# Performance work log

Hardware: AMD Instinct MI355X
Metric: run time of the kernel (lower is better)

## Reference

```python
import jax, jax.numpy as jnp
import numpy as np

EPSILON = 1e-8

def setup_inputs() -> dict:
    key = jax.random.key(0)
    k1, k2, k3, k4 = jax.random.split(key, 4)
    B, C_in, C_out, H, W, S, K = 16, 512, 512, 32, 32, 512, 3
    x = jax.random.normal(k1, (B, C_in, H, W), dtype=jnp.float32)
    w = jax.random.normal(k2, (B, S), dtype=jnp.float32)
    # Linear(style_dim -> in_chan), bias initialized to ones per module code
    style_w = jax.random.normal(k3, (C_in, S), dtype=jnp.float32) * (1.0 / np.sqrt(S))
    style_b = jnp.ones((C_in,), dtype=jnp.float32)
    # kaiming_normal_(fan_in, leaky_relu): std = sqrt(2/(1+0.01^2)) / sqrt(fan_in)
    fan_in = C_in * K * K
    gain = np.sqrt(2.0 / (1.0 + 0.01 ** 2))
    weight = jax.random.normal(k4, (C_out, C_in, K, K), dtype=jnp.float32) * (gain / np.sqrt(fan_in))
    return {"x": x, "w": w, "style_w": style_w, "style_b": style_b, "weight": weight}

def reference(x, w, style_w, style_b, weight):
    B, C, H, W_ = x.shape
    C_out, _, K, _ = weight.shape
    # style modulation: Linear(style_dim -> in_chan)
    style = w @ style_w.T + style_b                       # (B, C_in)
    weights = style[:, None, :, None, None] * weight[None]  # (B, C_out, C_in, K, K)
    # demodulation
    d = jax.lax.rsqrt(jnp.sum(weights * weights, axis=(2, 3, 4), keepdims=True) + EPSILON)
    weights = weights * d
    # grouped conv with groups = batch
    pad = 1 if K > 1 else 0
    xg = x.reshape(1, B * C, H, W_)
    wg = weights.reshape(B * C_out, C, K, K)
    y = jax.lax.conv_general_dilated(
        xg, wg, window_strides=(1, 1), padding=((pad, pad), (pad, pad)),
        dimension_numbers=("NCHW", "OIHW", "NCHW"), feature_group_count=B)
    return y.reshape(B, C_out, H, W_)
```

## Files before the change

kernel.cpp:

```cpp
#include <hip/hip_runtime.h>
#include <hip/hip_bf16.h>

#define NB 16
#define CI 512
#define CO 512
#define HW 1024
#define SD 512
#define EPSI 1e-8f

typedef __attribute__((ext_vector_type(8))) short bf16x8;
typedef __attribute__((ext_vector_type(16))) float f32x16;
typedef __attribute__((ext_vector_type(4))) unsigned int u32x4;

#define GLOAD_LDS16(g, l) __builtin_amdgcn_global_load_lds( \
    (const __attribute__((address_space(1))) unsigned int*)(const void*)(g), \
    (__attribute__((address_space(3))) unsigned int*)(void*)(l), 16, 0, 0)
#define SCHED0() __builtin_amdgcn_sched_barrier(0)
#define SBAR()   __builtin_amdgcn_s_barrier()

__global__ void k_style2(const float* __restrict__ w, const float* __restrict__ sw,
                         const float* __restrict__ sb, float* __restrict__ style) {
    int gw = (blockIdx.x * 256 + threadIdx.x) >> 6;
    int l = threadIdx.x & 63;
    int b = gw >> 9, c = gw & 511;
    const float4* wr = (const float4*)(w + b * SD) + (l << 1);
    const float4* sr = (const float4*)(sw + c * SD) + (l << 1);
    float4 a0 = wr[0], a1 = wr[1], q0 = sr[0], q1 = sr[1];
    float acc = a0.x * q0.x + a0.y * q0.y + a0.z * q0.z + a0.w * q0.w
              + a1.x * q1.x + a1.y * q1.y + a1.z * q1.z + a1.w * q1.w;
#pragma unroll
    for (int off = 32; off > 0; off >>= 1) acc += __shfl_down(acc, off);
    if (l == 0) style[gw] = acc + sb[c];
}

__global__ void k_wprep(const float* __restrict__ wt, float* __restrict__ wsq,
                        __hip_bfloat16* __restrict__ wtb, u32x4* __restrict__ zpage) {
    if (blockIdx.x == 0 && threadIdx.x < 64)
        zpage[threadIdx.x] = (u32x4){0, 0, 0, 0};
    int idx = blockIdx.x * 256 + threadIdx.x;
    const float* p = wt + idx * 9;
    float a = 0.f;
#pragma unroll
    for (int t = 0; t < 9; ++t) {
        float v = p[t];
        a += v * v;
        wtb[t * (CO * CI) + idx] = __float2bfloat16(v);
    }
    wsq[idx] = a;
}

__global__ void k_demod2(const float* __restrict__ style, const float* __restrict__ wsq,
                         float* __restrict__ dv) {
    int gw = (blockIdx.x * 256 + threadIdx.x) >> 6;
    int l = threadIdx.x & 63;
    int b = gw >> 9, co = gw & 511;
    const float4* st = (const float4*)(style + b * CI) + (l << 1);
    const float4* wq = (const float4*)(wsq + co * CI) + (l << 1);
    float4 s0 = st[0], s1 = st[1], q0 = wq[0], q1 = wq[1];
    float acc = s0.x * s0.x * q0.x + s0.y * s0.y * q0.y + s0.z * s0.z * q0.z + s0.w * s0.w * q0.w
              + s1.x * s1.x * q1.x + s1.y * s1.y * q1.y + s1.z * s1.z * q1.z + s1.w * s1.w * q1.w;
#pragma unroll
    for (int off = 32; off > 0; off >>= 1) acc += __shfl_down(acc, off);
    if (l == 0) dv[gw] = rsqrtf(acc + EPSI);
}

__global__ void k_xs(const float* __restrict__ x, const float* __restrict__ style,
                     __hip_bfloat16* __restrict__ xs) {
    __shared__ float tile[32][33];
    int b = blockIdx.z, c0 = blockIdx.y * 32, p0 = blockIdx.x * 32;
    int tx = threadIdx.x & 31, ty = threadIdx.x >> 5;
#pragma unroll
    for (int i = 0; i < 4; ++i) {
        int ci = c0 + ty + i * 8;
        tile[ty + i * 8][tx] = x[(b * CI + ci) * HW + p0 + tx] * style[b * CI + ci];
    }
    __syncthreads();
#pragma unroll
    for (int i = 0; i < 4; ++i) {
        int p = p0 + ty + i * 8;
        xs[(b * HW + p) * CI + c0 + tx] = __float2bfloat16(tile[tx][ty + i * 8]);
    }
}

#define XS_BYTES 26112
#define WBUF_BYTES 16384
#define SMEM_TOTAL (XS_BYTES + 3 * WBUF_BYTES)

extern "C" __global__ __launch_bounds__(256, 2) void k_conv(
        const __hip_bfloat16* __restrict__ wtb,
        const __hip_bfloat16* __restrict__ xs,
        const float* __restrict__ dvec,
        const char* __restrict__ zpage,
        float* __restrict__ out) {
    extern __shared__ char smem[];
    char* Xs  = smem;
    char* Wsb = smem + XS_BYTES;

    const int tid  = threadIdx.x;
    const int lane = tid & 63;
    const int wv   = tid >> 6;
    const int wr   = wv >> 1;
    const int wn   = wv & 1;

    int bid = blockIdx.x;
    int xcd = bid & 7, idx = bid >> 3;
    const int cot = xcd >> 1;
    const int px8 = idx & 7;
    const int b   = (idx >> 3) | ((xcd & 1) << 3);
    const int co0 = cot * 128;
    const int p0  = px8 * 128;
    const int y0  = px8 * 4;

    if (tid < 96) {
        int g = tid & 7;
        int rx = (tid & 8) ? 33 : 0;
        int row = tid >> 4;
        *(u32x4*)(Xs + (row * 34 + rx) * 128 + g * 16) = (u32x4){0, 0, 0, 0};
    }

    const int srcgW = (lane & 7) ^ (lane >> 3);

    auto issueW = [&](int tap, int cin, int bufi) {
        const __hip_bfloat16* wsrc = wtb + ((size_t)tap * CO + co0) * CI + cin;
        char* wdst = Wsb + bufi * WBUF_BYTES;
#pragma unroll
        for (int k = 0; k < 4; ++k) {
            int seg = k * 4 + wv;
            int co_l = seg * 8 + (lane >> 3);
            GLOAD_LDS16(wsrc + co_l * CI + srcgW * 8, wdst + seg * 1024);
        }
    };
    auto issueX = [&](int cin) {
#pragma unroll
        for (int k = 0; k < 6; ++k) {
            int sid = k * 4 + wv;
            int ry = sid >> 2, seg = sid & 3;
            int rx0 = 1 + seg * 8;
            char* ldst = Xs + (ry * 34 + rx0) * 128;
            int y = y0 - 1 + ry;
            int rx = rx0 + (lane >> 3);
            int srcg = (lane & 7) ^ (rx & 7);
            if ((unsigned)y < 32u)
                GLOAD_LDS16(xs + ((size_t)b * HW + (y << 5) + (rx - 1)) * CI + cin + srcg * 8, ldst);
            else
                GLOAD_LDS16(zpage, ldst);
        }
    };

    f32x16 acc[2][2];
#pragma unroll
    for (int m = 0; m < 2; ++m)
#pragma unroll
        for (int n = 0; n < 2; ++n)
            acc[m][n] = (f32x16)(0.f);

    issueW(0, 0, 0);
    issueW(1, 0, 1);
    issueX(0);
    SCHED0();
    asm volatile("s_waitcnt lgkmcnt(0) vmcnt(0)" ::: "memory");
    SCHED0();
    SBAR();
    SCHED0();

    for (int cc = 0; cc < 8; ++cc) {
#pragma unroll
        for (int t = 0; t < 9; ++t) {
            if (!(cc == 7 && t >= 7)) {
                const int tn  = (t <= 6) ? (t + 2) : (t - 7);
                const int cin = ((t <= 6) ? cc : (cc + 1)) * 64;
                issueW(tn, cin, (t + 2) % 3);
            }
            SCHED0();

            const char* Wb = Wsb + (t % 3) * WBUF_BYTES;
            const int ky = t / 3, kx = t - (t / 3) * 3;
            __builtin_amdgcn_s_setprio(1);
#pragma unroll
            for (int q = 0; q < 4; ++q) {
                bf16x8 afr[2], bfr[2];
                int g = (q << 1) + (lane >> 5);
#pragma unroll
                for (int m = 0; m < 2; ++m) {
                    int cr = wr * 64 + m * 32 + (lane & 31);
                    afr[m] = *(const bf16x8*)(Wb + cr * 128 + ((g ^ (cr & 7)) << 4));
                }
#pragma unroll
                for (int n = 0; n < 2; ++n) {
                    int ry = wn * 2 + n + ky;
                    int rx = (lane & 31) + kx;
                    bfr[n] = *(const bf16x8*)(Xs + ((ry * 34 + rx) * 128) +
                                              ((g ^ (rx & 7)) << 4));
                }
#pragma unroll
                for (int m = 0; m < 2; ++m)
#pragma unroll
                    for (int n = 0; n < 2; ++n)
                        acc[m][n] = __builtin_amdgcn_mfma_f32_32x32x16_bf16(afr[m], bfr[n], acc[m][n], 0, 0, 0);
            }
            __builtin_amdgcn_s_setprio(0);

            if (cc == 7 && t == 8) {
            } else if (t == 8) {
                SCHED0();
                asm volatile("s_waitcnt lgkmcnt(0)" ::: "memory");
                SCHED0();
                SBAR();
                SCHED0();
                issueX((cc + 1) * 64);
                SCHED0();
                asm volatile("s_waitcnt lgkmcnt(0) vmcnt(0)" ::: "memory");
                SCHED0();
                SBAR();
                SCHED0();
            } else if (cc == 7 && t == 7) {
                SCHED0();
                asm volatile("s_waitcnt lgkmcnt(0) vmcnt(0)" ::: "memory");
                SCHED0();
                SBAR();
                SCHED0();
            } else {
                SCHED0();
                asm volatile("s_waitcnt lgkmcnt(0) vmcnt(4)" ::: "memory");
                SCHED0();
                SBAR();
                SCHED0();
            }
        }
    }

#pragma unroll
    for (int m = 0; m < 2; ++m) {
#pragma unroll
        for (int r = 0; r < 16; ++r) {
            int co = co0 + wr * 64 + m * 32 + (r & 3) + ((r >> 2) << 3) + ((lane >> 5) << 2);
            float dvv = dvec[b * CO + co];
            float* orow = out + ((size_t)b * CO + co) * HW + p0 + wn * 64;
            orow[lane & 31]        = acc[m][0][r] * dvv;
            orow[32 + (lane & 31)] = acc[m][1][r] * dvv;
        }
    }
}

extern "C" void kernel_launch(void* const* d_in, const int* in_sizes, int n_in,
                              void* d_out, int out_size, void* d_ws, size_t ws_size,
                              hipStream_t stream) {
    const float* x  = (const float*)d_in[0];
    const float* w  = (const float*)d_in[1];
    const float* sw = (const float*)d_in[2];
    const float* sb = (const float*)d_in[3];
    const float* wt = (const float*)d_in[4];
    float* out = (float*)d_out;

    char* ws = (char*)d_ws;
    float* style = (float*)(ws);
    float* dvec  = (float*)(ws + 32768);
    float* wsq   = (float*)(ws + 65536);
    __hip_bfloat16* wtb = (__hip_bfloat16*)(ws + 1114112);
    __hip_bfloat16* xsb = (__hip_bfloat16*)(ws + 5832704);
    char* zpage = ws + 22609920;

    hipFuncSetAttribute((const void*)k_conv,
                        hipFuncAttributeMaxDynamicSharedMemorySize, SMEM_TOTAL);

    k_style2<<<2048, 256, 0, stream>>>(w, sw, sb, style);
    k_wprep<<<1024, 256, 0, stream>>>(wt, wsq, (__hip_bfloat16*)wtb, (u32x4*)zpage);
    k_xs<<<dim3(32, 16, 16), 256, 0, stream>>>(x, style, xsb);
    k_demod2<<<2048, 256, 0, stream>>>(style, wsq, dvec);
    k_conv<<<512, 256, SMEM_TOTAL, stream>>>(wtb, xsb, dvec, zpage, out);
}
```

Baseline: 99.90 us.

## Fuse demodulation into conv, split K across waves, widen xs transpose

Drops the separate demod kernel and computes the per-output-channel demod factors inside the conv prologue into LDS. The conv's wave decomposition changes from a 2x2 M/N split to a split of the K dimension across wave pairs, with a final LDS reduction before the store. The pipeline schedule is restructured so the X tile load is issued at the start of each channel chunk. The xs transpose kernel now handles 64 channels per block and writes 16-byte vectors. These changes aim to cut a kernel launch and increase A-fragment reuse per wave, at the cost of more accumulator registers and an extra reduction pass.

```diff
diff --git a/kernel.cpp b/kernel.cpp
--- a/kernel.cpp
+++ b/kernel.cpp
@@ -49,58 +49,48 @@
     wsq[idx] = a;
 }
 
-__global__ void k_demod2(const float* __restrict__ style, const float* __restrict__ wsq,
-                         float* __restrict__ dv) {
-    int gw = (blockIdx.x * 256 + threadIdx.x) >> 6;
-    int l = threadIdx.x & 63;
-    int b = gw >> 9, co = gw & 511;
-    const float4* st = (const float4*)(style + b * CI) + (l << 1);
-    const float4* wq = (const float4*)(wsq + co * CI) + (l << 1);
-    float4 s0 = st[0], s1 = st[1], q0 = wq[0], q1 = wq[1];
-    float acc = s0.x * s0.x * q0.x + s0.y * s0.y * q0.y + s0.z * s0.z * q0.z + s0.w * s0.w * q0.w
-              + s1.x * s1.x * q1.x + s1.y * s1.y * q1.y + s1.z * s1.z * q1.z + s1.w * s1.w * q1.w;
-#pragma unroll
-    for (int off = 32; off > 0; off >>= 1) acc += __shfl_down(acc, off);
-    if (l == 0) dv[gw] = rsqrtf(acc + EPSI);
-}
-
 __global__ void k_xs(const float* __restrict__ x, const float* __restrict__ style,
                      __hip_bfloat16* __restrict__ xs) {
-    __shared__ float tile[32][33];
-    int b = blockIdx.z, c0 = blockIdx.y * 32, p0 = blockIdx.x * 32;
+    __shared__ float tile[32][66];
+    int b = blockIdx.z, c0 = blockIdx.y * 64, p0 = blockIdx.x * 32;
     int tx = threadIdx.x & 31, ty = threadIdx.x >> 5;
 #pragma unroll
-    for (int i = 0; i < 4; ++i) {
-        int ci = c0 + ty + i * 8;
-        tile[ty + i * 8][tx] = x[(b * CI + ci) * HW + p0 + tx] * style[b * CI + ci];
+    for (int i = 0; i < 8; ++i) {
+        int ci = i * 8 + ty;
+        tile[tx][ci] = x[((size_t)b * CI + c0 + ci) * HW + p0 + tx] * style[b * CI + c0 + ci];
     }
     __syncthreads();
-#pragma unroll
-    for (int i = 0; i < 4; ++i) {
-        int p = p0 + ty + i * 8;
-        xs[(b * HW + p) * CI + c0 + tx] = __float2bfloat16(tile[tx][ty + i * 8]);
-    }
+    int r = threadIdx.x >> 3, kc = threadIdx.x & 7;
+    union { bf16x8 v; __hip_bfloat16 h[8]; } U;
+#pragma unroll
+    for (int i = 0; i < 8; ++i)
+        U.h[i] = __float2bfloat16(tile[r][kc * 8 + i]);
+    *(bf16x8*)(xs + ((size_t)b * HW + p0 + r) * CI + c0 + kc * 8) = U.v;
 }
 
 #define XS_BYTES 26112
-#define WBUF_BYTES 16384
-#define SMEM_TOTAL (XS_BYTES + 3 * WBUF_BYTES)
+#define WBUF 16384
+#define DV_OFF (XS_BYTES + 3 * WBUF)
+#define SMEM_TOTAL (DV_OFF + 512)
 
 extern "C" __global__ __launch_bounds__(256, 2) void k_conv(
         const __hip_bfloat16* __restrict__ wtb,
         const __hip_bfloat16* __restrict__ xs,
-        const float* __restrict__ dvec,
+        const float* __restrict__ style,
+        const float* __restrict__ wsq,
         const char* __restrict__ zpage,
         float* __restrict__ out) {
     extern __shared__ char smem[];
     char* Xs  = smem;
     char* Wsb = smem + XS_BYTES;
+    float* dvLDS = (float*)(smem + DV_OFF);
 
     const int tid  = threadIdx.x;
     const int lane = tid & 63;
+    const int l31  = lane & 31;
     const int wv   = tid >> 6;
-    const int wr   = wv >> 1;
-    const int wn   = wv & 1;
+    const int kh   = wv & 1;
+    const int wpx  = wv >> 1;
 
     int bid = blockIdx.x;
     int xcd = bid & 7, idx = bid >> 3;
@@ -122,20 +112,20 @@
 
     auto issueW = [&](int tap, int cin, int bufi) {
         const __hip_bfloat16* wsrc = wtb + ((size_t)tap * CO + co0) * CI + cin;
-        char* wdst = Wsb + bufi * WBUF_BYTES;
+        char* wdst = Wsb + bufi * WBUF;
 #pragma unroll
         for (int k = 0; k < 4; ++k) {
-            int seg = k * 4 + wv;
-            int co_l = seg * 8 + (lane >> 3);
-            GLOAD_LDS16(wsrc + co_l * CI + srcgW * 8, wdst + seg * 1024);
+            int u = k * 4 + wv;
+            int co_l = u * 8 + (lane >> 3);
+            GLOAD_LDS16(wsrc + co_l * CI + srcgW * 8, wdst + u * 1024);
         }
     };
     auto issueX = [&](int cin) {
 #pragma unroll
         for (int k = 0; k < 6; ++k) {
-            int sid = k * 4 + wv;
-            int ry = sid >> 2, seg = sid & 3;
-            int rx0 = 1 + seg * 8;
+            int u = k * 4 + wv;
+            int ry = u >> 2, q4 = u & 3;
+            int rx0 = 1 + q4 * 8;
             char* ldst = Xs + (ry * 34 + rx0) * 128;
             int y = y0 - 1 + ry;
             int rx = rx0 + (lane >> 3);
@@ -147,9 +137,9 @@
         }
     };
 
-    f32x16 acc[2][2];
-#pragma unroll
-    for (int m = 0; m < 2; ++m)
+    f32x16 acc[4][2];
+#pragma unroll
+    for (int m = 0; m < 4; ++m)
 #pragma unroll
         for (int n = 0; n < 2; ++n)
             acc[m][n] = (f32x16)(0.f);
@@ -157,6 +147,19 @@
     issueW(0, 0, 0);
     issueW(1, 0, 1);
     issueX(0);
+    {
+        int j = tid >> 1, h = tid & 1;
+        const float4* wq = (const float4*)(wsq + (size_t)(co0 + j) * CI + h * 256);
+        const float4* st = (const float4*)(style + b * CI + h * 256);
+        float a = 0.f;
+#pragma unroll 4
+        for (int i = 0; i < 64; ++i) {
+            float4 q = wq[i], s = st[i];
+            a += s.x * s.x * q.x + s.y * s.y * q.y + s.z * s.z * q.z + s.w * s.w * q.w;
+        }
+        a += __shfl_down(a, 1);
+        if (!h) dvLDS[j] = rsqrtf(a + EPSI);
+    }
     SCHED0();
     asm volatile("s_waitcnt lgkmcnt(0) vmcnt(0)" ::: "memory");
     SCHED0();
@@ -166,78 +169,101 @@
     for (int cc = 0; cc < 8; ++cc) {
 #pragma unroll
         for (int t = 0; t < 9; ++t) {
-            if (!(cc == 7 && t >= 7)) {
-                const int tn  = (t <= 6) ? (t + 2) : (t - 7);
-                const int cin = ((t <= 6) ? cc : (cc + 1)) * 64;
-                issueW(tn, cin, (t + 2) % 3);
-            }
-            SCHED0();
-
-            const char* Wb = Wsb + (t % 3) * WBUF_BYTES;
-            const int ky = t / 3, kx = t - (t / 3) * 3;
-            __builtin_amdgcn_s_setprio(1);
-#pragma unroll
-            for (int q = 0; q < 4; ++q) {
-                bf16x8 afr[2], bfr[2];
-                int g = (q << 1) + (lane >> 5);
-#pragma unroll
-                for (int m = 0; m < 2; ++m) {
-                    int cr = wr * 64 + m * 32 + (lane & 31);
-                    afr[m] = *(const bf16x8*)(Wb + cr * 128 + ((g ^ (cr & 7)) << 4));
-                }
-#pragma unroll
-                for (int n = 0; n < 2; ++n) {
-                    int ry = wn * 2 + n + ky;
-                    int rx = (lane & 31) + kx;
-                    bfr[n] = *(const bf16x8*)(Xs + ((ry * 34 + rx) * 128) +
-                                              ((g ^ (rx & 7)) << 4));
-                }
-#pragma unroll
-                for (int m = 0; m < 2; ++m)
-#pragma unroll
-                    for (int n = 0; n < 2; ++n)
-                        acc[m][n] = __builtin_amdgcn_mfma_f32_32x32x16_bf16(afr[m], bfr[n], acc[m][n], 0, 0, 0);
-            }
-            __builtin_amdgcn_s_setprio(0);
-
-            if (cc == 7 && t == 8) {
-            } else if (t == 8) {
-                SCHED0();
-                asm volatile("s_waitcnt lgkmcnt(0)" ::: "memory");
-                SCHED0();
-                SBAR();
-                SCHED0();
-                issueX((cc + 1) * 64);
-                SCHED0();
-                asm volatile("s_waitcnt lgkmcnt(0) vmcnt(0)" ::: "memory");
-                SCHED0();
-                SBAR();
-                SCHED0();
-            } else if (cc == 7 && t == 7) {
-                SCHED0();
-                asm volatile("s_waitcnt lgkmcnt(0) vmcnt(0)" ::: "memory");
-                SCHED0();
-                SBAR();
-                SCHED0();
-            } else {
+            const int s = cc * 9 + t;
+            if (t == 0 && cc > 0)
+                issueX(cc * 64);
+            if (s <= 69) {
+                const int s2 = s + 2;
+                issueW(s2 % 9, (s2 / 9) * 64, s2 % 3);
+            }
+            if (t == 0 && cc > 0) {
                 SCHED0();
                 asm volatile("s_waitcnt lgkmcnt(0) vmcnt(4)" ::: "memory");
                 SCHED0();
                 SBAR();
                 SCHED0();
             }
-        }
-    }
-
-#pragma unroll
-    for (int m = 0; m < 2; ++m) {
-#pragma unroll
-        for (int r = 0; r < 16; ++r) {
-            int co = co0 + wr * 64 + m * 32 + (r & 3) + ((r >> 2) << 3) + ((lane >> 5) << 2);
-            float dvv = dvec[b * CO + co];
-            float* orow = out + ((size_t)b * CO + co) * HW + p0 + wn * 64;
-            orow[lane & 31]        = acc[m][0][r] * dvv;
-            orow[32 + (lane & 31)] = acc[m][1][r] * dvv;
+
+            const char* Wb = Wsb + (t % 3) * WBUF;
+            const int ky = t / 3, kx = t - (t / 3) * 3;
+            __builtin_amdgcn_s_setprio(1);
+#pragma unroll
+            for (int ql = 0; ql < 2; ++ql) {
+                int g = kh * 4 + ql * 2 + (lane >> 5);
+                bf16x8 afr[4], bfr[2];
+#pragma unroll
+                for (int m = 0; m < 4; ++m) {
+                    int cr = m * 32 + l31;
+                    afr[m] = *(const bf16x8*)(Wb + cr * 128 + ((g ^ (cr & 7)) << 4));
+                }
+#pragma unroll
+                for (int n = 0; n < 2; ++n) {
+                    int row = wpx * 2 + n + ky;
+                    int rx = l31 + kx;
+                    bfr[n] = *(const bf16x8*)(Xs + (row * 34 + rx) * 128 + ((g ^ (rx & 7)) << 4));
+                }
+#pragma unroll
+                for (int m = 0; m < 4; ++m)
+#pragma unroll
+                    for (int n = 0; n < 2; ++n)
+                        acc[m][n] = __builtin_amdgcn_mfma_f32_32x32x16_bf16(afr[m], bfr[n], acc[m][n], 0, 0, 0);
+            }
+            __builtin_amdgcn_s_setprio(0);
+
+            SCHED0();
+            if (cc == 7 && t == 8) {
+                asm volatile("s_waitcnt lgkmcnt(0)" ::: "memory");
+            } else if (cc == 7 && t == 7) {
+                asm volatile("s_waitcnt lgkmcnt(0) vmcnt(0)" ::: "memory");
+            } else {
+                asm volatile("s_waitcnt lgkmcnt(0) vmcnt(4)" ::: "memory");
+            }
+            SCHED0();
+            SBAR();
+            SCHED0();
+        }
+    }
+
+    if (kh) {
+        char* rb = smem + wpx * 32768;
+#pragma unroll
+        for (int m = 0; m < 4; ++m)
+#pragma unroll
+            for (int n = 0; n < 2; ++n)
+#pragma unroll
+                for (int g4 = 0; g4 < 4; ++g4) {
+                    float4 v = make_float4(acc[m][n][g4 * 4 + 0], acc[m][n][g4 * 4 + 1],
+                                           acc[m][n][g4 * 4 + 2], acc[m][n][g4 * 4 + 3]);
+                    *(float4*)(rb + ((((m * 2 + n) * 4 + g4) * 64) + lane) * 16) = v;
+                }
+    }
+    SCHED0();
+    asm volatile("s_waitcnt lgkmcnt(0)" ::: "memory");
+    SCHED0();
+    SBAR();
+    SCHED0();
+    if (!kh) {
+        char* rb = smem + wpx * 32768;
+#pragma unroll
+        for (int m = 0; m < 4; ++m) {
+#pragma unroll
+            for (int n = 0; n < 2; ++n)
+#pragma unroll
+                for (int g4 = 0; g4 < 4; ++g4) {
+                    float4 v = *(const float4*)(rb + ((((m * 2 + n) * 4 + g4) * 64) + lane) * 16);
+                    acc[m][n][g4 * 4 + 0] += v.x;
+                    acc[m][n][g4 * 4 + 1] += v.y;
+                    acc[m][n][g4 * 4 + 2] += v.z;
+                    acc[m][n][g4 * 4 + 3] += v.w;
+                }
+#pragma unroll
+            for (int r = 0; r < 16; ++r) {
+                int col = m * 32 + (r & 3) + ((r >> 2) << 3) + ((lane >> 5) << 2);
+                float dvv = dvLDS[col];
+                float* orow = out + ((size_t)b * CO + co0 + col) * HW + p0 + wpx * 64;
+                orow[l31]      = acc[m][0][r] * dvv;
+                orow[32 + l31] = acc[m][1][r] * dvv;
+            }
         }
     }
 }
@@ -254,7 +280,6 @@
 
     char* ws = (char*)d_ws;
     float* style = (float*)(ws);
-    float* dvec  = (float*)(ws + 32768);
     float* wsq   = (float*)(ws + 65536);
     __hip_bfloat16* wtb = (__hip_bfloat16*)(ws + 1114112);
     __hip_bfloat16* xsb = (__hip_bfloat16*)(ws + 5832704);
@@ -265,7 +290,6 @@
 
     k_style2<<<2048, 256, 0, stream>>>(w, sw, sb, style);
     k_wprep<<<1024, 256, 0, stream>>>(wt, wsq, (__hip_bfloat16*)wtb, (u32x4*)zpage);
-    k_xs<<<dim3(32, 16, 16), 256, 0, stream>>>(x, style, xsb);
-    k_demod2<<<2048, 256, 0, stream>>>(style, wsq, dvec);
-    k_conv<<<512, 256, SMEM_TOTAL, stream>>>(wtb, xsb, dvec, zpage, out);
-}
+    k_xs<<<dim3(32, 8, 16), 256, 0, stream>>>(x, style, xsb);
+    k_conv<<<512, 256, SMEM_TOTAL, stream>>>(wtb, xsb, style, wsq, zpage, out);
+}
```

After: 115.7 us. 1.16x slower.
